# Kernel optimization log

Hardware: AMD Instinct MI355X
Metric: run time of the kernel (lower is better)

Reference implementation:

```python
import jax, jax.numpy as jnp
import numpy as np

B, N, H, D = 8, 2048, 4, 64  # batch, seq, heads (multi_head_count), head_dim
OUT = 256


def setup_inputs() -> dict:
    key = jax.random.key(0)
    ks = jax.random.split(key, 9)
    s = 0.02
    return {
        "x": jax.random.normal(ks[0], (B, N, H * D), dtype=jnp.float32),
        "Wq": jax.random.normal(ks[1], (H, D, D), dtype=jnp.float32) * s,
        "Wk": jax.random.normal(ks[2], (H, D, D), dtype=jnp.float32) * s,
        "Wv": jax.random.normal(ks[3], (H, D, D), dtype=jnp.float32) * s,
        "bq": jnp.zeros((H, D), dtype=jnp.float32),
        "bk": jnp.zeros((H, D), dtype=jnp.float32),
        "bv": jnp.zeros((H, D), dtype=jnp.float32),
        "Wp": jax.random.normal(ks[4], (H * D, OUT), dtype=jnp.float32) * s,
        "bp": jnp.zeros((OUT,), dtype=jnp.float32),
    }


def reference(x, Wq, Wk, Wv, bq, bk, bv, Wp, bp):
    # x: [b, n, h*d] -> [b, h, n, d]
    b, n, _ = x.shape
    xh = x.reshape(b, n, H, D).transpose(0, 2, 1, 3)
    # per-head Q/K/V with per-head weights (heads selected = [0..H-1], deterministic for num_heads==4)
    q = jnp.einsum("bhnd,hde->bhne", xh, Wq) + bq[None, :, None, :]
    k = jnp.einsum("bhnd,hde->bhne", xh, Wk) + bk[None, :, None, :]
    v = jnp.einsum("bhnd,hde->bhne", xh, Wv) + bv[None, :, None, :]
    scale = 1.0 / jnp.sqrt(jnp.asarray(D, dtype=x.dtype))
    scores = jnp.einsum("bhne,bhme->bhnm", q, k) * scale  # [b,h,n,n]
    attn = jax.nn.softmax(scores, axis=-1)
    o = jnp.einsum("bhnm,bhme->bhne", attn, v)  # [b,h,n,d]
    # concat heads: [b, n, h*d], then final projection
    o = o.transpose(0, 2, 1, 3).reshape(b, n, H * D)
    return o @ Wp + bp
```

## Files before the change

kernel.cpp:

```cpp
#include <hip/hip_runtime.h>

typedef __attribute__((ext_vector_type(4)))  float  f32x4;
typedef __attribute__((ext_vector_type(16))) float  f32x16;
typedef __attribute__((ext_vector_type(8)))  __bf16 bf16x8;
typedef __attribute__((ext_vector_type(2)))  unsigned u32x2;

constexpr int Bv = 8, Nv = 2048, Hv = 4, Dv = 64, OUTv = 256, HD = 256;
constexpr int BH = Bv * Hv;
constexpr size_t PH = (size_t)BH * Nv * Dv;

#if __has_builtin(__builtin_amdgcn_exp2f)
#define EXP2(x) __builtin_amdgcn_exp2f(x)
#else
#define EXP2(x) exp2f(x)
#endif

__device__ __forceinline__ unsigned short f2bf(float f) {
    union { __bf16 h; unsigned short u; } r;
    r.h = (__bf16)f;
    return r.u;
}

__device__ __forceinline__ unsigned pk_bf16(float a, float b) {
    union { __bf16 h[2]; unsigned u; } r;
    r.h[0] = (__bf16)a; r.h[1] = (__bf16)b;
    return r.u;
}

__device__ __forceinline__ uint4 pack8(const float* f) {
    uint4 u;
    u.x = pk_bf16(f[0], f[1]);
    u.y = pk_bf16(f[2], f[3]);
    u.z = pk_bf16(f[4], f[5]);
    u.w = pk_bf16(f[6], f[7]);
    return u;
}

__device__ __forceinline__ void swap32(unsigned a, unsigned b, unsigned& lo, unsigned& hi) {
#if __has_builtin(__builtin_amdgcn_permlane32_swap)
    u32x2 r = __builtin_amdgcn_permlane32_swap(a, b, false, false);
    lo = r.x; hi = r.y;
#else
    const int ishi = (threadIdx.x & 63) >> 5;
    unsigned pa = __shfl_xor(a, 32, 64), pb = __shfl_xor(b, 32, 64);
    lo = ishi ? pb : a;
    hi = ishi ? b : pa;
#endif
}

#define GLOBAL_AS __attribute__((address_space(1)))
#define LDS_AS    __attribute__((address_space(3)))

__global__ __launch_bounds__(256) void wconv_kernel(
    const float* __restrict__ Wq, const float* __restrict__ Wk, const float* __restrict__ Wv,
    const float* __restrict__ Wp,
    unsigned short* __restrict__ Wt3, unsigned short* __restrict__ Wpt)
{
    const int idx = blockIdx.x * 256 + threadIdx.x;
    if (idx < 49152) {
        const int m = idx >> 14, r = idx & 16383;
        const int h = r >> 12, e = (r >> 6) & 63, d = r & 63;
        const float* W = (m == 0) ? Wq : ((m == 1) ? Wk : Wv);
        Wt3[idx] = f2bf(W[(h << 12) + d * 64 + e]);
    } else {
        const int r = idx - 49152;
        const int e = r >> 8, c = r & 255;
        Wpt[r] = f2bf(Wp[c * 256 + e]);
    }
}

__global__ __launch_bounds__(256) void qkv_kernel(
    const float* __restrict__ x,
    const unsigned short* __restrict__ Wt3,
    const float* __restrict__ bq, const float* __restrict__ bk, const float* __restrict__ bv,
    unsigned short* __restrict__ Qb, unsigned short* __restrict__ Kb,
    unsigned short* __restrict__ Vt)
{
    const int h = blockIdx.x & 3;
    const int tt = blockIdx.x >> 2;
    const int tok0 = tt * 64;
    const int t = threadIdx.x, l = t & 63, w = t >> 6;
    const int lg = l >> 4, lc = l & 15;

    __shared__ uint4 Xs[64 * 8];
    __shared__ uint4 Ws[3 * 512];
    __shared__ uint4 Os[64 * 8];

#pragma unroll
    for (int k = 0; k < 6; ++k) {
        const int s = k * 256 + t;
        const int m = s >> 9, sm = s & 511;
        const int e = sm >> 3, cp = sm & 7;
        __builtin_amdgcn_global_load_lds(
            (const GLOBAL_AS unsigned int*)(Wt3 + (m << 14) + (h << 12) + (e << 6) + ((cp ^ (e & 7)) << 3)),
            (LDS_AS unsigned int*)((char*)Ws + (k * 256 + w * 64) * 16),
            16, 0, 0);
    }

    {
        const int r = t >> 2, c4 = t & 3;
        const float* src = x + (size_t)(tok0 + r) * HD + h * Dv + c4 * 16;
        float f[16];
        *(float4*)(f)      = *(const float4*)(src);
        *(float4*)(f + 4)  = *(const float4*)(src + 4);
        *(float4*)(f + 8)  = *(const float4*)(src + 8);
        *(float4*)(f + 12) = *(const float4*)(src + 12);
        Xs[r * 8 + ((c4 * 2)     ^ (r & 7))] = pack8(f);
        Xs[r * 8 + ((c4 * 2 + 1) ^ (r & 7))] = pack8(f + 8);
    }
    asm volatile("s_waitcnt vmcnt(0)" ::: "memory");
    __syncthreads();

    const int ar = w * 16 + lc;
    bf16x8 a[2];
    a[0] = ((const bf16x8*)Xs)[ar * 8 + (lg       ^ (ar & 7))];
    a[1] = ((const bf16x8*)Xs)[ar * 8 + ((4 + lg) ^ (ar & 7))];

    f32x4 acc[3][4];
#pragma unroll
    for (int m = 0; m < 3; ++m)
#pragma unroll
        for (int nt = 0; nt < 4; ++nt) acc[m][nt] = (f32x4){0.f, 0.f, 0.f, 0.f};

#pragma unroll
    for (int kk = 0; kk < 2; ++kk) {
#pragma unroll
        for (int m = 0; m < 3; ++m) {
#pragma unroll
            for (int nt = 0; nt < 4; ++nt) {
                const int br = nt * 16 + lc;
                const bf16x8 b = ((const bf16x8*)Ws)[(m << 9) + br * 8 + ((kk * 4 + lg) ^ (br & 7))];
                acc[m][nt] = __builtin_amdgcn_mfma_f32_16x16x32_bf16(a[kk], b, acc[m][nt], 0, 0, 0);
            }
        }
    }

    const int b_ = tok0 >> 11, n_ = tok0 & (Nv - 1);
    const int bh = b_ * Hv + h;
    const float QSCALE = 0.125f * 1.44269504088896340736f;

    __syncthreads();
    {
        unsigned short* Os16 = (unsigned short*)Os;
        unsigned short* Ks16 = (unsigned short*)Xs;
        unsigned short* Vs16 = (unsigned short*)Ws;
#pragma unroll
        for (int nt = 0; nt < 4; ++nt) {
            const int e = nt * 16 + lc;
            const float bq_ = bq[h * Dv + e];
            const float bk_ = bk[h * Dv + e];
            const float bv_ = bv[h * Dv + e];
#pragma unroll
            for (int j = 0; j < 4; ++j) {
                const int row = w * 16 + lg * 4 + j;
                const int ch = (e >> 3) ^ (row & 7);
                Os16[row * 64 + ch * 8 + (e & 7)] = f2bf((acc[0][nt][j] + bq_) * QSCALE);
                Ks16[row * 64 + ch * 8 + (e & 7)] = f2bf(acc[1][nt][j] + bk_);
                const int chv = (row >> 3) ^ (e & 7);
                Vs16[e * 64 + chv * 8 + (row & 7)] = f2bf(acc[2][nt][j] + bv_);
            }
        }
    }
    __syncthreads();
    {
        const int r = t >> 2, c4 = t & 3;
        unsigned short* dq = Qb + ((size_t)bh * Nv + n_ + r) * Dv + c4 * 16;
        *(uint4*)dq       = Os[r * 8 + ((c4 * 2)     ^ (r & 7))];
        *(uint4*)(dq + 8) = Os[r * 8 + ((c4 * 2 + 1) ^ (r & 7))];
        unsigned short* dk = Kb + ((size_t)bh * Nv + n_ + r) * Dv + c4 * 16;
        *(uint4*)dk       = Xs[r * 8 + ((c4 * 2)     ^ (r & 7))];
        *(uint4*)(dk + 8) = Xs[r * 8 + ((c4 * 2 + 1) ^ (r & 7))];
        unsigned short* dv = Vt + ((size_t)bh * Dv + r) * Nv + n_ + c4 * 16;
        *(uint4*)dv       = Ws[r * 8 + ((c4 * 2)     ^ (r & 7))];
        *(uint4*)(dv + 8) = Ws[r * 8 + ((c4 * 2 + 1) ^ (r & 7))];
    }
}

__global__ __launch_bounds__(256, 2) void attn_kernel(
    const unsigned short* __restrict__ Qb, const unsigned short* __restrict__ Kb,
    const unsigned short* __restrict__ Vt, unsigned short* __restrict__ Ob)
{
    const int bh = blockIdx.x & 31;
    const int qt = blockIdx.x >> 5;
    const int t = threadIdx.x, w = t >> 6, l = t & 63;
    const int hi = l >> 5, lc = l & 31;

    __shared__ uint4 Ks[2][128 * 8];
    __shared__ uint4 Vs[2][64 * 16];

    const unsigned short* Kg = Kb + (size_t)bh * Nv * Dv;
    const unsigned short* Vg = Vt + (size_t)bh * Dv * Nv;

    const int q_ = qt * 128 + w * 32 + lc;
    const unsigned short* Qrow = Qb + ((size_t)bh * Nv + q_) * Dv;
    bf16x8 qf[4];
#pragma unroll
    for (int kk = 0; kk < 4; ++kk)
        qf[kk] = *(const bf16x8*)(Qrow + kk * 16 + hi * 8);

    bf16x8 onesf;
#pragma unroll
    for (int i = 0; i < 8; ++i) onesf[i] = (__bf16)1.0f;

    auto stage = [&](int buf, int kt) {
#pragma unroll
        for (int k = 0; k < 4; ++k) {
            const int s = k * 256 + t;
            const int base = k * 256 + w * 64;
            {
                const int r = s >> 3, c = (s & 7) ^ (r & 7);
                __builtin_amdgcn_global_load_lds(
                    (const GLOBAL_AS unsigned int*)(Kg + ((size_t)kt * 128 + r) * Dv + c * 8),
                    (LDS_AS unsigned int*)((char*)&Ks[buf][0] + base * 16),
                    16, 0, 0);
            }
            {
                const int r = s >> 4, c = (s & 15) ^ (r & 15);
                __builtin_amdgcn_global_load_lds(
                    (const GLOBAL_AS unsigned int*)(Vg + (size_t)r * Nv + kt * 128 + c * 8),
                    (LDS_AS unsigned int*)((char*)&Vs[buf][0] + base * 16),
                    16, 0, 0);
            }
        }
    };

    f32x16 o0, o1, o2, z16;
#pragma unroll
    for (int i = 0; i < 16; ++i) { o0[i] = 0.f; o1[i] = 0.f; o2[i] = 0.f; z16[i] = 0.f; }

    stage(0, 0);
    asm volatile("s_waitcnt vmcnt(0)" ::: "memory");
    __syncthreads();

    int cur = 0;
    for (int kt = 0; kt < Nv / 128; ++kt) {
        if (kt < Nv / 128 - 1) stage(cur ^ 1, kt + 1);

        const uint4* KsB = &Ks[cur][0];
        const uint4* VsB = &Vs[cur][0];

        f32x16 s4[4];
        __builtin_amdgcn_s_setprio(1);
#pragma unroll
        for (int nt = 0; nt < 4; ++nt) {
            const int r = nt * 32 + lc;
            const bf16x8 af = *(const bf16x8*)&KsB[r * 8 + (hi ^ (r & 7))];
            s4[nt] = __builtin_amdgcn_mfma_f32_32x32x16_bf16(af, qf[0], z16, 0, 0, 0);
        }
#pragma unroll
        for (int kk = 1; kk < 4; ++kk) {
#pragma unroll
            for (int nt = 0; nt < 4; ++nt) {
                const int r = nt * 32 + lc;
                const bf16x8 af = *(const bf16x8*)&KsB[r * 8 + ((kk * 2 + hi) ^ (r & 7))];
                s4[nt] = __builtin_amdgcn_mfma_f32_32x32x16_bf16(af, qf[kk], s4[nt], 0, 0, 0);
            }
        }
        __builtin_amdgcn_s_setprio(0);

#pragma unroll
        for (int nt = 0; nt < 4; ++nt) {
#pragma unroll
            for (int r = 0; r < 16; ++r) s4[nt][r] = EXP2(s4[nt][r]);

            unsigned c[8];
#pragma unroll
            for (int i = 0; i < 8; ++i) c[i] = pk_bf16(s4[nt][2 * i], s4[nt][2 * i + 1]);

            unsigned d0a, d2a, d1a, d3a, d0b, d2b, d1b, d3b;
            swap32(c[0], c[2], d0a, d2a);
            swap32(c[1], c[3], d1a, d3a);
            swap32(c[4], c[6], d0b, d2b);
            swap32(c[5], c[7], d1b, d3b);

            union { unsigned u[4]; bf16x8 v; } pf0, pf1;
            pf0.u[0] = d0a; pf0.u[1] = d1a; pf0.u[2] = d2a; pf0.u[3] = d3a;
            pf1.u[0] = d0b; pf1.u[1] = d1b; pf1.u[2] = d2b; pf1.u[3] = d3b;

            __builtin_amdgcn_s_setprio(1);
#pragma unroll
            for (int kslow = 0; kslow < 2; ++kslow) {
                const bf16x8 pf = kslow ? pf1.v : pf0.v;
                {
                    const int row = lc;
                    const int ch = (nt * 4 + kslow * 2 + hi) ^ (row & 15);
                    const bf16x8 vf = *(const bf16x8*)&VsB[row * 16 + ch];
                    o0 = __builtin_amdgcn_mfma_f32_32x32x16_bf16(vf, pf, o0, 0, 0, 0);
                }
                {
                    const int row = 32 + lc;
                    const int ch = (nt * 4 + kslow * 2 + hi) ^ (row & 15);
                    const bf16x8 vf = *(const bf16x8*)&VsB[row * 16 + ch];
                    o1 = __builtin_amdgcn_mfma_f32_32x32x16_bf16(vf, pf, o1, 0, 0, 0);
                }
                o2 = __builtin_amdgcn_mfma_f32_32x32x16_bf16(onesf, pf, o2, 0, 0, 0);
            }
            __builtin_amdgcn_s_setprio(0);
        }

        if (kt < Nv / 128 - 1) {
            asm volatile("s_waitcnt vmcnt(0)" ::: "memory");
            __syncthreads();
            cur ^= 1;
        }
    }

    const float inv = 1.0f / o2[0];
    const int b_ = bh >> 2, h_ = bh & 3;
    unsigned short* orow = Ob + ((size_t)b_ * Nv + q_) * HD + h_ * Dv;
#pragma unroll
    for (int g = 0; g < 4; ++g) {
        uint2 ua, ub;
        ua.x = pk_bf16(o0[g * 4 + 0] * inv, o0[g * 4 + 1] * inv);
        ua.y = pk_bf16(o0[g * 4 + 2] * inv, o0[g * 4 + 3] * inv);
        ub.x = pk_bf16(o1[g * 4 + 0] * inv, o1[g * 4 + 1] * inv);
        ub.y = pk_bf16(o1[g * 4 + 2] * inv, o1[g * 4 + 3] * inv);
        *(uint2*)(orow + 8 * g + 4 * hi)      = ua;
        *(uint2*)(orow + 32 + 8 * g + 4 * hi) = ub;
    }
}

__global__ __launch_bounds__(256) void proj_kernel(
    const unsigned short* __restrict__ Ob, const unsigned short* __restrict__ Wpt,
    const float* __restrict__ bp, float* __restrict__ out)
{
    const int tok0 = blockIdx.x * 32;
    const int t = threadIdx.x, w = t >> 6, l = t & 63;
    const int hi = l >> 5, lc = l & 31;

    __shared__ uint4 SH[2][2304];

    auto stage = [&](int buf, int kt) {
        const int c0 = kt * 64;
#pragma unroll
        for (int j = 0; j < 9; ++j) {
            const int s = j * 256 + t;
            const int base = j * 256 + w * 64;
            if (s < 256) {
                const int r = s >> 3, cp = s & 7;
                __builtin_amdgcn_global_load_lds(
                    (const GLOBAL_AS unsigned int*)(Ob + (size_t)(tok0 + r) * HD + c0 + ((cp ^ (r & 7)) << 3)),
                    (LDS_AS unsigned int*)((char*)&SH[buf][0] + base * 16),
                    16, 0, 0);
            } else {
                const int s2 = s - 256;
                const int e = s2 >> 3, cp = s2 & 7;
                __builtin_amdgcn_global_load_lds(
                    (const GLOBAL_AS unsigned int*)(Wpt + (size_t)e * HD + c0 + ((cp ^ (e & 7)) << 3)),
                    (LDS_AS unsigned int*)((char*)&SH[buf][0] + base * 16),
                    16, 0, 0);
            }
        }
    };

    f32x16 acc[2];
#pragma unroll
    for (int ct = 0; ct < 2; ++ct)
#pragma unroll
        for (int i = 0; i < 16; ++i) acc[ct][i] = 0.f;

    stage(0, 0);
    for (int kt = 0; kt < 4; ++kt) {
        if (kt < 3) {
            stage((kt + 1) & 1, kt + 1);
            asm volatile("s_waitcnt vmcnt(9)" ::: "memory");
        } else {
            asm volatile("s_waitcnt vmcnt(0)" ::: "memory");
        }
        __syncthreads();

        const bf16x8* Osh = (const bf16x8*)&SH[kt & 1][0];
        const bf16x8* Wsh = (const bf16x8*)&SH[kt & 1][256];
#pragma unroll
        for (int kk = 0; kk < 4; ++kk) {
            const bf16x8 af = Osh[lc * 8 + ((kk * 2 + hi) ^ (lc & 7))];
#pragma unroll
            for (int ct = 0; ct < 2; ++ct) {
                const int e = w * 64 + ct * 32 + lc;
                const bf16x8 bf_ = Wsh[e * 8 + ((kk * 2 + hi) ^ (e & 7))];
                acc[ct] = __builtin_amdgcn_mfma_f32_32x32x16_bf16(af, bf_, acc[ct], 0, 0, 0);
            }
        }
        __syncthreads();
    }

#pragma unroll
    for (int ct = 0; ct < 2; ++ct) {
        const int e = w * 64 + ct * 32 + lc;
        const float bias = bp[e];
#pragma unroll
        for (int r = 0; r < 16; ++r) {
            const int tok = tok0 + (r & 3) + 8 * (r >> 2) + 4 * hi;
            out[(size_t)tok * OUTv + e] = acc[ct][r] + bias;
        }
    }
}

extern "C" void kernel_launch(void* const* d_in, const int* in_sizes, int n_in,
                              void* d_out, int out_size, void* d_ws, size_t ws_size,
                              hipStream_t stream)
{
    const float* x  = (const float*)d_in[0];
    const float* Wq = (const float*)d_in[1];
    const float* Wk = (const float*)d_in[2];
    const float* Wv = (const float*)d_in[3];
    const float* bq = (const float*)d_in[4];
    const float* bk = (const float*)d_in[5];
    const float* bv = (const float*)d_in[6];
    const float* Wp = (const float*)d_in[7];
    const float* bp = (const float*)d_in[8];
    float* out = (float*)d_out;

    unsigned short* us = (unsigned short*)d_ws;
    unsigned short* Qb  = us;
    unsigned short* Kb  = us + PH;
    unsigned short* Vt  = us + 2 * PH;
    unsigned short* Ob  = us + 3 * PH;
    unsigned short* Wt3 = us + 4 * PH;
    unsigned short* Wpt = Wt3 + 49152;

    wconv_kernel<<<448, 256, 0, stream>>>(Wq, Wk, Wv, Wp, Wt3, Wpt);
    qkv_kernel<<<(Bv * Nv / 64) * Hv, 256, 0, stream>>>(x, Wt3, bq, bk, bv, Qb, Kb, Vt);
    attn_kernel<<<(Nv / 128) * BH, 256, 0, stream>>>(Qb, Kb, Vt, Ob);
    proj_kernel<<<Bv * Nv / 32, 256, 0, stream>>>(Ob, Wpt, bp, out);
}
```

Measured before the change: 146.4 us.

## Enlarge token tiles in qkv and proj kernels, tile-transpose weight conversion

The qkv kernel now handles 128 tokens per block instead of 64, so each staged weight tile is reused across two row groups of MFMAs. The proj kernel handles 64 tokens per block with 4 output tiles per wave, which halves the number of times Wp is reloaded. The weight conversion kernel now transposes through an LDS tile with coalesced loads and stores, replacing scattered per-element reads. In exchange there are fewer blocks (less parallelism), more LDS per block, and higher register pressure.

```diff
diff --git a/kernel.cpp b/kernel.cpp
--- a/kernel.cpp
+++ b/kernel.cpp
@@ -56,16 +56,54 @@
     const float* __restrict__ Wp,
     unsigned short* __restrict__ Wt3, unsigned short* __restrict__ Wpt)
 {
-    const int idx = blockIdx.x * 256 + threadIdx.x;
-    if (idx < 49152) {
-        const int m = idx >> 14, r = idx & 16383;
-        const int h = r >> 12, e = (r >> 6) & 63, d = r & 63;
+    __shared__ unsigned short tile[64 * 64];
+    const int t = threadIdx.x;
+    const int bid = blockIdx.x;
+
+    const float* src;
+    unsigned short* dst;
+    int src_ld, dst_ld;
+    if (bid < 12) {
+        const int m = bid >> 2, h = bid & 3;
         const float* W = (m == 0) ? Wq : ((m == 1) ? Wk : Wv);
-        Wt3[idx] = f2bf(W[(h << 12) + d * 64 + e]);
+        src = W + (h << 12);
+        dst = Wt3 + (m << 14) + (h << 12);
+        src_ld = 64; dst_ld = 64;
     } else {
-        const int r = idx - 49152;
-        const int e = r >> 8, c = r & 255;
-        Wpt[r] = f2bf(Wp[c * 256 + e]);
+        const int b2 = bid - 12;
+        const int er = b2 >> 2, cr = b2 & 3;
+        src = Wp + (size_t)(cr * 64) * OUTv + er * 64;
+        dst = Wpt + (size_t)(er * 64) * HD + cr * 64;
+        src_ld = OUTv; dst_ld = HD;
+    }
+
+    {
+        const int r = t >> 2, c0 = (t & 3) * 16;
+        const float* s = src + (size_t)r * src_ld + c0;
+        float f[16];
+        *(float4*)(f)      = *(const float4*)(s);
+        *(float4*)(f + 4)  = *(const float4*)(s + 4);
+        *(float4*)(f + 8)  = *(const float4*)(s + 8);
+        *(float4*)(f + 12) = *(const float4*)(s + 12);
+#pragma unroll
+        for (int i = 0; i < 16; ++i)
+            tile[r * 64 + ((c0 + i + r) & 63)] = f2bf(f[i]);
+    }
+    __syncthreads();
+    {
+        const int e = t >> 2, d0 = (t & 3) * 16;
+        unsigned v[8];
+#pragma unroll
+        for (int p = 0; p < 8; ++p) {
+            const int da = d0 + 2 * p, db = da + 1;
+            const unsigned lo = tile[da * 64 + ((e + da) & 63)];
+            const unsigned hi = tile[db * 64 + ((e + db) & 63)];
+            v[p] = lo | (hi << 16);
+        }
+        uint4* d16 = (uint4*)(dst + (size_t)e * dst_ld + d0);
+        uint4 o0; o0.x = v[0]; o0.y = v[1]; o0.z = v[2]; o0.w = v[3];
+        uint4 o1; o1.x = v[4]; o1.y = v[5]; o1.z = v[6]; o1.w = v[7];
+        d16[0] = o0; d16[1] = o1;
     }
 }
 
@@ -78,13 +116,13 @@
 {
     const int h = blockIdx.x & 3;
     const int tt = blockIdx.x >> 2;
-    const int tok0 = tt * 64;
+    const int tok0 = tt * 128;
     const int t = threadIdx.x, l = t & 63, w = t >> 6;
     const int lg = l >> 4, lc = l & 15;
 
-    __shared__ uint4 Xs[64 * 8];
+    __shared__ uint4 Xs[128 * 8];
     __shared__ uint4 Ws[3 * 512];
-    __shared__ uint4 Os[64 * 8];
+    __shared__ uint4 Os[128 * 8];
 
 #pragma unroll
     for (int k = 0; k < 6; ++k) {
@@ -98,29 +136,34 @@
     }
 
     {
-        const int r = t >> 2, c4 = t & 3;
-        const float* src = x + (size_t)(tok0 + r) * HD + h * Dv + c4 * 16;
-        float f[16];
-        *(float4*)(f)      = *(const float4*)(src);
-        *(float4*)(f + 4)  = *(const float4*)(src + 4);
-        *(float4*)(f + 8)  = *(const float4*)(src + 8);
-        *(float4*)(f + 12) = *(const float4*)(src + 12);
-        Xs[r * 8 + ((c4 * 2)     ^ (r & 7))] = pack8(f);
-        Xs[r * 8 + ((c4 * 2 + 1) ^ (r & 7))] = pack8(f + 8);
+        const int r = t >> 1, hf = t & 1;
+        const float* src = x + (size_t)(tok0 + r) * HD + h * Dv + hf * 32;
+        float f[32];
+#pragma unroll
+        for (int p = 0; p < 8; ++p)
+            *(float4*)(f + p * 4) = *(const float4*)(src + p * 4);
+#pragma unroll
+        for (int p = 0; p < 4; ++p)
+            Xs[r * 8 + ((hf * 4 + p) ^ (r & 7))] = pack8(f + p * 8);
     }
     asm volatile("s_waitcnt vmcnt(0)" ::: "memory");
     __syncthreads();
 
-    const int ar = w * 16 + lc;
-    bf16x8 a[2];
-    a[0] = ((const bf16x8*)Xs)[ar * 8 + (lg       ^ (ar & 7))];
-    a[1] = ((const bf16x8*)Xs)[ar * 8 + ((4 + lg) ^ (ar & 7))];
-
-    f32x4 acc[3][4];
+    bf16x8 a[2][2];
+#pragma unroll
+    for (int rg = 0; rg < 2; ++rg) {
+        const int ar = w * 32 + rg * 16 + lc;
+        a[rg][0] = ((const bf16x8*)Xs)[ar * 8 + (lg       ^ (ar & 7))];
+        a[rg][1] = ((const bf16x8*)Xs)[ar * 8 + ((4 + lg) ^ (ar & 7))];
+    }
+
+    f32x4 acc[3][2][4];
 #pragma unroll
     for (int m = 0; m < 3; ++m)
 #pragma unroll
-        for (int nt = 0; nt < 4; ++nt) acc[m][nt] = (f32x4){0.f, 0.f, 0.f, 0.f};
+        for (int rg = 0; rg < 2; ++rg)
+#pragma unroll
+            for (int nt = 0; nt < 4; ++nt) acc[m][rg][nt] = (f32x4){0.f, 0.f, 0.f, 0.f};
 
 #pragma unroll
     for (int kk = 0; kk < 2; ++kk) {
@@ -130,7 +173,9 @@
             for (int nt = 0; nt < 4; ++nt) {
                 const int br = nt * 16 + lc;
                 const bf16x8 b = ((const bf16x8*)Ws)[(m << 9) + br * 8 + ((kk * 4 + lg) ^ (br & 7))];
-                acc[m][nt] = __builtin_amdgcn_mfma_f32_16x16x32_bf16(a[kk], b, acc[m][nt], 0, 0, 0);
+#pragma unroll
+                for (int rg = 0; rg < 2; ++rg)
+                    acc[m][rg][nt] = __builtin_amdgcn_mfma_f32_16x16x32_bf16(a[rg][kk], b, acc[m][rg][nt], 0, 0, 0);
             }
         }
     }
@@ -151,28 +196,39 @@
             const float bk_ = bk[h * Dv + e];
             const float bv_ = bv[h * Dv + e];
 #pragma unroll
-            for (int j = 0; j < 4; ++j) {
-                const int row = w * 16 + lg * 4 + j;
-                const int ch = (e >> 3) ^ (row & 7);
-                Os16[row * 64 + ch * 8 + (e & 7)] = f2bf((acc[0][nt][j] + bq_) * QSCALE);
-                Ks16[row * 64 + ch * 8 + (e & 7)] = f2bf(acc[1][nt][j] + bk_);
-                const int chv = (row >> 3) ^ (e & 7);
-                Vs16[e * 64 + chv * 8 + (row & 7)] = f2bf(acc[2][nt][j] + bv_);
+            for (int rg = 0; rg < 2; ++rg) {
+#pragma unroll
+                for (int j = 0; j < 4; ++j) {
+                    const int row = w * 32 + rg * 16 + lg * 4 + j;
+                    const int ch = (e >> 3) ^ (row & 7);
+                    Os16[row * 64 + ch * 8 + (e & 7)] = f2bf((acc[0][rg][nt][j] + bq_) * QSCALE);
+                    Ks16[row * 64 + ch * 8 + (e & 7)] = f2bf(acc[1][rg][nt][j] + bk_);
+                    const int cv = row >> 3;
+                    const int pv = ((cv ^ e) & 7) | (cv & 8);
+                    Vs16[e * 128 + pv * 8 + (row & 7)] = f2bf(acc[2][rg][nt][j] + bv_);
+                }
             }
         }
     }
     __syncthreads();
     {
-        const int r = t >> 2, c4 = t & 3;
-        unsigned short* dq = Qb + ((size_t)bh * Nv + n_ + r) * Dv + c4 * 16;
-        *(uint4*)dq       = Os[r * 8 + ((c4 * 2)     ^ (r & 7))];
-        *(uint4*)(dq + 8) = Os[r * 8 + ((c4 * 2 + 1) ^ (r & 7))];
-        unsigned short* dk = Kb + ((size_t)bh * Nv + n_ + r) * Dv + c4 * 16;
-        *(uint4*)dk       = Xs[r * 8 + ((c4 * 2)     ^ (r & 7))];
-        *(uint4*)(dk + 8) = Xs[r * 8 + ((c4 * 2 + 1) ^ (r & 7))];
-        unsigned short* dv = Vt + ((size_t)bh * Dv + r) * Nv + n_ + c4 * 16;
-        *(uint4*)dv       = Ws[r * 8 + ((c4 * 2)     ^ (r & 7))];
-        *(uint4*)(dv + 8) = Ws[r * 8 + ((c4 * 2 + 1) ^ (r & 7))];
+        const int r = t >> 1, cq = (t & 1) * 4;
+        unsigned short* dq = Qb + ((size_t)bh * Nv + n_ + r) * Dv;
+        unsigned short* dk = Kb + ((size_t)bh * Nv + n_ + r) * Dv;
+#pragma unroll
+        for (int i = 0; i < 4; ++i) {
+            const int ch = cq + i;
+            *(uint4*)(dq + ch * 8) = Os[r * 8 + (ch ^ (r & 7))];
+            *(uint4*)(dk + ch * 8) = Xs[r * 8 + (ch ^ (r & 7))];
+        }
+        const int e = t >> 2, cv0 = (t & 3) * 4;
+        unsigned short* dv = Vt + ((size_t)bh * Dv + e) * Nv + n_;
+#pragma unroll
+        for (int i = 0; i < 4; ++i) {
+            const int c = cv0 + i;
+            const int pv = ((c ^ e) & 7) | (c & 8);
+            *(uint4*)(dv + c * 8) = Ws[e * 16 + pv];
+        }
     }
 }
 
@@ -324,26 +380,27 @@
     const unsigned short* __restrict__ Ob, const unsigned short* __restrict__ Wpt,
     const float* __restrict__ bp, float* __restrict__ out)
 {
-    const int tok0 = blockIdx.x * 32;
+    const int tok0 = blockIdx.x * 64;
     const int t = threadIdx.x, w = t >> 6, l = t & 63;
     const int hi = l >> 5, lc = l & 31;
-
-    __shared__ uint4 SH[2][2304];
+    const int tw = w >> 1;
+
+    __shared__ uint4 SH[2][2560];
 
     auto stage = [&](int buf, int kt) {
         const int c0 = kt * 64;
 #pragma unroll
-        for (int j = 0; j < 9; ++j) {
+        for (int j = 0; j < 10; ++j) {
             const int s = j * 256 + t;
             const int base = j * 256 + w * 64;
-            if (s < 256) {
+            if (s < 512) {
                 const int r = s >> 3, cp = s & 7;
                 __builtin_amdgcn_global_load_lds(
                     (const GLOBAL_AS unsigned int*)(Ob + (size_t)(tok0 + r) * HD + c0 + ((cp ^ (r & 7)) << 3)),
                     (LDS_AS unsigned int*)((char*)&SH[buf][0] + base * 16),
                     16, 0, 0);
             } else {
-                const int s2 = s - 256;
+                const int s2 = s - 512;
                 const int e = s2 >> 3, cp = s2 & 7;
                 __builtin_amdgcn_global_load_lds(
                     (const GLOBAL_AS unsigned int*)(Wpt + (size_t)e * HD + c0 + ((cp ^ (e & 7)) << 3)),
@@ -353,9 +410,9 @@
         }
     };
 
-    f32x16 acc[2];
-#pragma unroll
-    for (int ct = 0; ct < 2; ++ct)
+    f32x16 acc[4];
+#pragma unroll
+    for (int ct = 0; ct < 4; ++ct)
 #pragma unroll
         for (int i = 0; i < 16; ++i) acc[ct][i] = 0.f;
 
@@ -363,20 +420,21 @@
     for (int kt = 0; kt < 4; ++kt) {
         if (kt < 3) {
             stage((kt + 1) & 1, kt + 1);
-            asm volatile("s_waitcnt vmcnt(9)" ::: "memory");
+            asm volatile("s_waitcnt vmcnt(10)" ::: "memory");
         } else {
             asm volatile("s_waitcnt vmcnt(0)" ::: "memory");
         }
         __syncthreads();
 
         const bf16x8* Osh = (const bf16x8*)&SH[kt & 1][0];
-        const bf16x8* Wsh = (const bf16x8*)&SH[kt & 1][256];
+        const bf16x8* Wsh = (const bf16x8*)&SH[kt & 1][512];
+        const int r = tw * 32 + lc;
 #pragma unroll
         for (int kk = 0; kk < 4; ++kk) {
-            const bf16x8 af = Osh[lc * 8 + ((kk * 2 + hi) ^ (lc & 7))];
-#pragma unroll
-            for (int ct = 0; ct < 2; ++ct) {
-                const int e = w * 64 + ct * 32 + lc;
+            const bf16x8 af = Osh[r * 8 + ((kk * 2 + hi) ^ (r & 7))];
+#pragma unroll
+            for (int ct = 0; ct < 4; ++ct) {
+                const int e = (w & 1) * 128 + ct * 32 + lc;
                 const bf16x8 bf_ = Wsh[e * 8 + ((kk * 2 + hi) ^ (e & 7))];
                 acc[ct] = __builtin_amdgcn_mfma_f32_32x32x16_bf16(af, bf_, acc[ct], 0, 0, 0);
             }
@@ -385,12 +443,12 @@
     }
 
 #pragma unroll
-    for (int ct = 0; ct < 2; ++ct) {
-        const int e = w * 64 + ct * 32 + lc;
+    for (int ct = 0; ct < 4; ++ct) {
+        const int e = (w & 1) * 128 + ct * 32 + lc;
         const float bias = bp[e];
 #pragma unroll
         for (int r = 0; r < 16; ++r) {
-            const int tok = tok0 + (r & 3) + 8 * (r >> 2) + 4 * hi;
+            const int tok = tok0 + tw * 32 + (r & 3) + 8 * (r >> 2) + 4 * hi;
             out[(size_t)tok * OUTv + e] = acc[ct][r] + bias;
         }
     }
@@ -419,8 +477,8 @@
     unsigned short* Wt3 = us + 4 * PH;
     unsigned short* Wpt = Wt3 + 49152;
 
-    wconv_kernel<<<448, 256, 0, stream>>>(Wq, Wk, Wv, Wp, Wt3, Wpt);
-    qkv_kernel<<<(Bv * Nv / 64) * Hv, 256, 0, stream>>>(x, Wt3, bq, bk, bv, Qb, Kb, Vt);
+    wconv_kernel<<<28, 256, 0, stream>>>(Wq, Wk, Wv, Wp, Wt3, Wpt);
+    qkv_kernel<<<(Bv * Nv / 128) * Hv, 256, 0, stream>>>(x, Wt3, bq, bk, bv, Qb, Kb, Vt);
     attn_kernel<<<(Nv / 128) * BH, 256, 0, stream>>>(Qb, Kb, Vt, Ob);
-    proj_kernel<<<Bv * Nv / 32, 256, 0, stream>>>(Ob, Wpt, bp, out);
-}
+    proj_kernel<<<Bv * Nv / 64, 256, 0, stream>>>(Ob, Wpt, bp, out);
+}
```

Measured after the change: 149.5 us. 1.02x slower.
